# Optimization experiments

Hardware: AMD Instinct MI355X
Metric: run time of the kernel (lower is better)

The kernel has to match this reference:

```python
import jax, jax.numpy as jnp
import numpy as np

INV_SQRT3 = 0.5773502691896258  # e3nn wigner_3j entries for (0,1,1),(1,0,1),(1,1,0)


def setup_inputs() -> dict:
    key = jax.random.key(0)
    ks = jax.random.split(key, 9)
    B, N = 2, 256
    d_in, m1 = 256, 1          # input irreps: d_in x0e + m1 x1o
    d_h, m5, m3 = 256, 5, 3    # hidden irreps: d_h x0e + 5 x1o + 3 x1o
    d_out = 2                  # output irreps: 2 x0e
    return {
        "vectors": jax.random.normal(ks[0], (B, N, 3 * m1), jnp.float32),
        "scalars": jax.random.normal(ks[1], (B, N, d_in), jnp.float32),
        # e3nn internal weights ~ N(0,1); one weight block per CG path (uvw)
        "W1": jax.random.normal(ks[2], (d_in, d_in, d_h), jnp.float32),   # 0e x 0e -> 0e
        "W2a": jax.random.normal(ks[3], (d_in, m1, m5), jnp.float32),     # 0e x 1o -> 1o (mul 5)
        "W2b": jax.random.normal(ks[4], (d_in, m1, m3), jnp.float32),     # 0e x 1o -> 1o (mul 3)
        "W3a": jax.random.normal(ks[5], (m1, d_in, m5), jnp.float32),     # 1o x 0e -> 1o (mul 5)
        "W3b": jax.random.normal(ks[6], (m1, d_in, m3), jnp.float32),     # 1o x 0e -> 1o (mul 3)
        "W4": jax.random.normal(ks[7], (m1, m1, d_h), jnp.float32),       # 1o x 1o -> 0e
        "WL": jax.random.normal(ks[8], (d_h, d_out), jnp.float32),        # Linear d_h x0e -> 2 x0e
    }


def reference(vectors, scalars, W1, W2a, W2b, W3a, W3b, W4, WL):
    B, N, d = scalars.shape
    m1 = vectors.shape[-1] // 3
    z = B * N
    s = scalars.reshape(z, d)          # (z, d)  scalar (0e) channels
    v = vectors.reshape(z, m1, 3)      # (z, m1, 3)  vector (1o) channels
    d_h = W1.shape[-1]
    # e3nn FullyConnectedTensorProduct path weights ('component' irrep norm,
    # 'element' path norm): sqrt(ir_out.dim / sum_paths(mul1*mul2))
    pw0 = (1.0 / (d * d + m1 * m1)) ** 0.5      # into 0e output (paths 0e*0e and 1o*1o)
    pw1 = (3.0 / (2.0 * d * m1)) ** 0.5         # into each 1o output (paths 0e*1o and 1o*0e)
    # --- 0e x 0e -> 0e (dominant path) + 1o x 1o -> 0e ---
    t = jnp.einsum('zu,uvw->zvw', s, W1)        # (z, d, d_h)
    out0 = jnp.einsum('zv,zvw->zw', s, t)       # (z, d_h)
    out0 = out0 + INV_SQRT3 * jnp.einsum('zui,zvi,uvw->zw', v, v, W4)
    out0 = pw0 * out0
    # --- 0e x 1o -> 1o and 1o x 0e -> 1o (present in hidden irreps; they have
    # no path into the final 2x0e output, kept for structural fidelity) ---
    out1 = pw1 * INV_SQRT3 * (jnp.einsum('zu,zvk,uvw->zwk', s, v, W2a)
                              + jnp.einsum('zuk,zv,uvw->zwk', v, s, W3a))  # (z,5,3)
    out2 = pw1 * INV_SQRT3 * (jnp.einsum('zu,zvk,uvw->zwk', s, v, W2b)
                              + jnp.einsum('zuk,zv,uvw->zwk', v, s, W3b))  # (z,3,3)
    del out1, out2
    # --- e3nn Linear(hidden, 2x0e): only 0e->0e path, 1/sqrt(fan_in) norm ---
    lin = jnp.einsum('zu,uw->zw', out0, WL) / (d_h ** 0.5)   # (z, 2)
    m_eqv = lin[:, :1].reshape(B, N, 1)
    m_inv = lin[:, 1:].reshape(B, N, 1)
    return (m_eqv, m_inv)
```

## Files before the change

kernel.cpp:

```cpp
#include <hip/hip_runtime.h>


typedef __attribute__((ext_vector_type(8))) short bf16x8;
typedef __attribute__((ext_vector_type(4))) float f32x4;
typedef __attribute__((ext_vector_type(4))) int int4v;

#define LDS_S_BYTES 65536
#define LDS_B_PITCH 80
#define LDS_B_TILE (64 * LDS_B_PITCH)
#define LDS_TOTAL (LDS_S_BYTES + 2 * LDS_B_TILE)

__device__ __forceinline__ float bfbits2f(unsigned short h) {
  return __uint_as_float(((unsigned)h) << 16);
}
__device__ __forceinline__ unsigned pk2bf(float lo, float hi) {
  unsigned r;
  asm("v_cvt_pk_bf16_f32 %0, %1, %2" : "=v"(r) : "v"(lo), "v"(hi));
  return r;
}

__global__ __launch_bounds__(512) void eg_gemm(const float* __restrict__ s,
                                               const float* __restrict__ W1,
                                               float* __restrict__ out0) {
  extern __shared__ char smem[];
  char* sB0 = smem + LDS_S_BYTES;

  const int bx = blockIdx.x;
  const int nt = bx & 3;
  const int vc = (bx >> 2) & 7;
  const int uc = bx >> 5;
  const int u0 = uc * 32, v0 = vc * 32, w0 = nt * 64;

  const int tid = threadIdx.x;
  const int lane = tid & 63;
  const int wid = tid >> 6;
  const int l15 = lane & 15;
  const int g = lane >> 4;

  for (int j = 0; j < 16; ++j) {
    int id = j * 512 + tid;
    int z = id >> 4;
    int c4 = id & 15;
    int srccol = (c4 < 8) ? (u0 + (c4 << 2)) : (v0 + ((c4 - 8) << 2));
    const float4 f = *(const float4*)(s + z * 256 + srccol);
    unsigned p0 = pk2bf(f.x, f.y);
    unsigned p1 = pk2bf(f.z, f.w);
    int slot = c4 >> 1;
    char* dst = smem + z * 128 + (((slot ^ (z & 7)) << 4) | ((c4 & 1) << 3));
    *(unsigned*)dst = p0;
    *(unsigned*)(dst + 4) = p1;
  }

  const int vrow = tid >> 4;
  const int w4g = (tid & 15) << 2;
  const float* gsrc = W1 + (((u0 * 256) + v0 + vrow) * 256 + w0 + w4g);

  {
    float4 c0 = *(const float4*)(gsrc);
    unsigned q0 = pk2bf(c0.x, c0.y), q1 = pk2bf(c0.z, c0.w);
    char* base = sB0 + vrow * 2;
    *(unsigned short*)(base + (w4g + 0) * LDS_B_PITCH) = (unsigned short)(q0);
    *(unsigned short*)(base + (w4g + 1) * LDS_B_PITCH) = (unsigned short)(q0 >> 16);
    *(unsigned short*)(base + (w4g + 2) * LDS_B_PITCH) = (unsigned short)(q1);
    *(unsigned short*)(base + (w4g + 3) * LDS_B_PITCH) = (unsigned short)(q1 >> 16);
  }
  __syncthreads();

  f32x4 acc[4][4];
  #pragma unroll
  for (int a = 0; a < 4; ++a)
    #pragma unroll
    for (int b = 0; b < 4; ++b)
      acc[a][b] = 0.f;

  const int zb = wid * 64 + l15;
  const char* sbase = smem + zb * 128;
  const int svoff = ((4 + g) ^ (l15 & 7)) << 4;
  const int broff = l15 * LDS_B_PITCH + g * 16;

  for (int us = 0; us < 32; ++us) {
    float4 nx;
    if (us < 31) nx = *(const float4*)(gsrc + (us + 1) * 65536);

    const char* bt = sB0 + (us & 1) * LDS_B_TILE;

    bf16x8 afr[4];
    const int suoff = ((((us >> 3) ^ (l15 & 7)) << 4) | ((us & 7) << 1));
    #pragma unroll
    for (int mf = 0; mf < 4; ++mf) {
      const char* rowp = sbase + mf * 16 * 128;
      float su = bfbits2f(*(const unsigned short*)(rowp + suoff));
      int4v sv = *(const int4v*)(rowp + svoff);
      int4v af;
      #pragma unroll
      for (int jj = 0; jj < 4; ++jj) {
        unsigned p = (unsigned)sv[jj];
        float f0 = __uint_as_float(p << 16) * su;
        float f1 = __uint_as_float(p & 0xffff0000u) * su;
        af[jj] = (int)pk2bf(f0, f1);
      }
      afr[mf] = __builtin_bit_cast(bf16x8, af);
    }

    #pragma unroll
    for (int nf = 0; nf < 4; ++nf) {
      bf16x8 bfr = *(const bf16x8*)(bt + nf * 16 * LDS_B_PITCH + broff);
      #pragma unroll
      for (int mf = 0; mf < 4; ++mf) {
        acc[mf][nf] = __builtin_amdgcn_mfma_f32_16x16x32_bf16(afr[mf], bfr, acc[mf][nf], 0, 0, 0);
      }
    }

    if (us < 31) {
      char* btn = sB0 + ((us + 1) & 1) * LDS_B_TILE;
      unsigned q0 = pk2bf(nx.x, nx.y), q1 = pk2bf(nx.z, nx.w);
      char* base = btn + vrow * 2;
      *(unsigned short*)(base + (w4g + 0) * LDS_B_PITCH) = (unsigned short)(q0);
      *(unsigned short*)(base + (w4g + 1) * LDS_B_PITCH) = (unsigned short)(q0 >> 16);
      *(unsigned short*)(base + (w4g + 2) * LDS_B_PITCH) = (unsigned short)(q1);
      *(unsigned short*)(base + (w4g + 3) * LDS_B_PITCH) = (unsigned short)(q1 >> 16);
    }
    __syncthreads();
  }

  #pragma unroll
  for (int mf = 0; mf < 4; ++mf)
    #pragma unroll
    for (int nf = 0; nf < 4; ++nf)
      #pragma unroll
      for (int r = 0; r < 4; ++r) {
        int z = wid * 64 + mf * 16 + g * 4 + r;
        int w = w0 + nf * 16 + l15;
        atomicAdd(out0 + z * 256 + w, acc[mf][nf][r]);
      }
}

__global__ void eg_finish(const float* __restrict__ vec,
                          const float* __restrict__ W4,
                          const float* __restrict__ WL,
                          const float* __restrict__ acc,
                          float* __restrict__ out) {
  const int z = blockIdx.x;
  const int lane = threadIdx.x;
  float v0 = vec[z * 3 + 0], v1 = vec[z * 3 + 1], v2 = vec[z * 3 + 2];
  const float b = 0.57735026918962576f * (v0 * v0 + v1 * v1 + v2 * v2);
  float a0 = 0.f, a1 = 0.f;
  #pragma unroll
  for (int j = 0; j < 4; ++j) {
    int w = j * 64 + lane;
    float o = acc[z * 256 + w] + b * W4[w];
    a0 += o * WL[2 * w];
    a1 += o * WL[2 * w + 1];
  }
  #pragma unroll
  for (int off = 32; off > 0; off >>= 1) {
    a0 += __shfl_xor(a0, off);
    a1 += __shfl_xor(a1, off);
  }
  if (lane == 0) {
    out[z] = 2.4413876e-04f * a0;
    out[512 + z] = 2.4413876e-04f * a1;
  }
}

extern "C" void kernel_launch(void* const* d_in, const int* in_sizes, int n_in,
                              void* d_out, int out_size, void* d_ws, size_t ws_size,
                              hipStream_t stream) {
  const float* vectors = (const float*)d_in[0];
  const float* scalars = (const float*)d_in[1];
  const float* W1 = (const float*)d_in[2];
  const float* W4 = (const float*)d_in[7];
  const float* WL = (const float*)d_in[8];
  float* out = (float*)d_out;
  float* acc = (float*)d_ws;

  hipMemsetAsync(acc, 0, 512 * 256 * sizeof(float), stream);
  eg_gemm<<<256, 512, LDS_TOTAL, stream>>>(scalars, W1, acc);
  eg_finish<<<512, 64, 0, stream>>>(vectors, W4, WL, acc, out);
}
```

Baseline: 160.3 us.

## Switch GEMM to fp16, split z across blocks, deepen W1 prefetch pipeline

The kernel now converts operands to fp16 with round-toward-zero packing and uses f16 MFMA, so the per-step A-fragment scaling becomes packed half multiplies instead of unpack, fp32 multiply and repack. The grid goes from 256 blocks of 512 threads to 512 blocks of 256 threads, splitting z in two halves, which halves LDS per block and lets more blocks run per CU. W1 is prefetched two u-steps at a time through registers with a four-buffer LDS ring and swizzled vector writes, replacing the scattered 2-byte transposed stores, with a barrier every two steps instead of every step. fp16 products may lose range and precision, and each W1 tile is now loaded twice, once per z half.

```diff
diff --git a/kernel.cpp b/kernel.cpp
--- a/kernel.cpp
+++ b/kernel.cpp
@@ -1,137 +1,177 @@
 #include <hip/hip_runtime.h>
 
 
-typedef __attribute__((ext_vector_type(8))) short bf16x8;
+typedef __attribute__((ext_vector_type(8))) _Float16 f16x8;
+typedef __attribute__((ext_vector_type(2))) _Float16 f16x2;
 typedef __attribute__((ext_vector_type(4))) float f32x4;
+typedef __attribute__((ext_vector_type(2))) int int2v;
 typedef __attribute__((ext_vector_type(4))) int int4v;
 
-#define LDS_S_BYTES 65536
-#define LDS_B_PITCH 80
-#define LDS_B_TILE (64 * LDS_B_PITCH)
-#define LDS_TOTAL (LDS_S_BYTES + 2 * LDS_B_TILE)
-
-__device__ __forceinline__ float bfbits2f(unsigned short h) {
-  return __uint_as_float(((unsigned)h) << 16);
-}
-__device__ __forceinline__ unsigned pk2bf(float lo, float hi) {
-  unsigned r;
-  asm("v_cvt_pk_bf16_f32 %0, %1, %2" : "=v"(r) : "v"(lo), "v"(hi));
-  return r;
-}
-
-__global__ __launch_bounds__(512) void eg_gemm(const float* __restrict__ s,
-                                               const float* __restrict__ W1,
-                                               float* __restrict__ out0) {
+#define LDS_S 32768
+#define BP 80
+#define BSTEP 5120
+#define LDS_TOTAL (LDS_S + 4 * BSTEP)
+
+__device__ __forceinline__ unsigned pkrtz(float a, float b) {
+  return __builtin_bit_cast(unsigned, __builtin_amdgcn_cvt_pkrtz(a, b));
+}
+__device__ __forceinline__ int hbits(f16x2 h) {
+  return __builtin_bit_cast(int, h);
+}
+__device__ __forceinline__ void barrier_lds() {
+  asm volatile("s_waitcnt lgkmcnt(0)" ::: "memory");
+  __builtin_amdgcn_s_barrier();
+}
+
+__global__ __launch_bounds__(256, 3) void eg_gemm(const float* __restrict__ s,
+                                                  const float* __restrict__ W1,
+                                                  float* __restrict__ out0) {
   extern __shared__ char smem[];
-  char* sB0 = smem + LDS_S_BYTES;
+  char* sB = smem + LDS_S;
 
   const int bx = blockIdx.x;
-  const int nt = bx & 3;
-  const int vc = (bx >> 2) & 7;
-  const int uc = bx >> 5;
-  const int u0 = uc * 32, v0 = vc * 32, w0 = nt * 64;
-
-  const int tid = threadIdx.x;
-  const int lane = tid & 63;
-  const int wid = tid >> 6;
+  const int zh = bx >> 8;
+  const int uvw = bx & 255;
+  const int wt = uvw & 3, vc = (uvw >> 2) & 7, uc = uvw >> 5;
+  const int u0 = uc * 32, v0 = vc * 32, w0 = wt * 64;
+
+  const int t = threadIdx.x;
+  const int lane = t & 63;
+  const int wid = t >> 6;
   const int l15 = lane & 15;
   const int g = lane >> 4;
 
   for (int j = 0; j < 16; ++j) {
-    int id = j * 512 + tid;
-    int z = id >> 4;
+    int id = j * 256 + t;
+    int zl = id >> 4;
     int c4 = id & 15;
     int srccol = (c4 < 8) ? (u0 + (c4 << 2)) : (v0 + ((c4 - 8) << 2));
-    const float4 f = *(const float4*)(s + z * 256 + srccol);
-    unsigned p0 = pk2bf(f.x, f.y);
-    unsigned p1 = pk2bf(f.z, f.w);
+    const float4 f = *(const float4*)(s + (zh * 256 + zl) * 256 + srccol);
     int slot = c4 >> 1;
-    char* dst = smem + z * 128 + (((slot ^ (z & 7)) << 4) | ((c4 & 1) << 3));
-    *(unsigned*)dst = p0;
-    *(unsigned*)(dst + 4) = p1;
-  }
-
-  const int vrow = tid >> 4;
-  const int w4g = (tid & 15) << 2;
-  const float* gsrc = W1 + (((u0 * 256) + v0 + vrow) * 256 + w0 + w4g);
-
-  {
-    float4 c0 = *(const float4*)(gsrc);
-    unsigned q0 = pk2bf(c0.x, c0.y), q1 = pk2bf(c0.z, c0.w);
-    char* base = sB0 + vrow * 2;
-    *(unsigned short*)(base + (w4g + 0) * LDS_B_PITCH) = (unsigned short)(q0);
-    *(unsigned short*)(base + (w4g + 1) * LDS_B_PITCH) = (unsigned short)(q0 >> 16);
-    *(unsigned short*)(base + (w4g + 2) * LDS_B_PITCH) = (unsigned short)(q1);
-    *(unsigned short*)(base + (w4g + 3) * LDS_B_PITCH) = (unsigned short)(q1 >> 16);
-  }
-  __syncthreads();
+    char* dst = smem + zl * 128 + (((slot ^ (zl & 7)) << 4) | ((c4 & 1) << 3));
+    *(int2v*)dst = int2v{(int)pkrtz(f.x, f.y), (int)pkrtz(f.z, f.w)};
+  }
+
+  const int wB = t & 63;
+  const int vg = t >> 6;
+  const int hsw = (wB >> 3) & 7;
+  const int sl0 = (vg ^ hsw) << 3;
+  const int sl1 = ((vg + 4) ^ hsw) << 3;
+  const float* gB = W1 + (size_t)u0 * 65536 + (v0 + vg * 4) * 256 + w0 + wB;
+
+  float pa0, pa1, pa2, pa3, pa4, pa5, pa6, pa7;
+  float pb0, pb1, pb2, pb3, pb4, pb5, pb6, pb7;
+
+#define ISSUE(usbase)                                                       \
+  do {                                                                      \
+    const float* q0_ = gB + (size_t)(usbase) * 65536;                       \
+    pa0 = q0_[0];    pa1 = q0_[256];      pa2 = q0_[512];  pa3 = q0_[768];  \
+    pa4 = q0_[4096]; pa5 = q0_[4096+256]; pa6 = q0_[4096+512];              \
+    pa7 = q0_[4096+768];                                                    \
+    const float* q1_ = q0_ + 65536;                                         \
+    pb0 = q1_[0];    pb1 = q1_[256];      pb2 = q1_[512];  pb3 = q1_[768];  \
+    pb4 = q1_[4096]; pb5 = q1_[4096+256]; pb6 = q1_[4096+512];              \
+    pb7 = q1_[4096+768];                                                    \
+  } while (0)
+
+#define WRITEPF(dst0_)                                                       \
+  do {                                                                       \
+    char* d0_ = (dst0_);                                                     \
+    *(int2v*)(d0_ + wB * BP + sl0) =                                         \
+        int2v{(int)pkrtz(pa0, pa1), (int)pkrtz(pa2, pa3)};                   \
+    *(int2v*)(d0_ + wB * BP + sl1) =                                         \
+        int2v{(int)pkrtz(pa4, pa5), (int)pkrtz(pa6, pa7)};                   \
+    char* d1_ = d0_ + BSTEP;                                                 \
+    *(int2v*)(d1_ + wB * BP + sl0) =                                         \
+        int2v{(int)pkrtz(pb0, pb1), (int)pkrtz(pb2, pb3)};                   \
+    *(int2v*)(d1_ + wB * BP + sl1) =                                         \
+        int2v{(int)pkrtz(pb4, pb5), (int)pkrtz(pb6, pb7)};                   \
+  } while (0)
+
+  ISSUE(0);
+  WRITEPF(sB);
+  ISSUE(2);
+  barrier_lds();
+
+  const int swz = l15 & 7;
+  int4v sv[4];
+#pragma unroll
+  for (int mf = 0; mf < 4; ++mf) {
+    const char* p = smem + (wid * 64 + mf * 16 + l15) * 128 + (((4 + g) ^ swz) << 4);
+    sv[mf] = *(const int4v*)p;
+  }
+
+  int baddr[4];
+#pragma unroll
+  for (int nf = 0; nf < 4; ++nf) {
+    int w = nf * 16 + l15;
+    baddr[nf] = w * BP + (((2 * g) ^ ((w >> 3) & 7)) << 3);
+  }
 
   f32x4 acc[4][4];
-  #pragma unroll
+#pragma unroll
   for (int a = 0; a < 4; ++a)
-    #pragma unroll
-    for (int b = 0; b < 4; ++b)
-      acc[a][b] = 0.f;
-
-  const int zb = wid * 64 + l15;
-  const char* sbase = smem + zb * 128;
-  const int svoff = ((4 + g) ^ (l15 & 7)) << 4;
-  const int broff = l15 * LDS_B_PITCH + g * 16;
-
-  for (int us = 0; us < 32; ++us) {
-    float4 nx;
-    if (us < 31) nx = *(const float4*)(gsrc + (us + 1) * 65536);
-
-    const char* bt = sB0 + (us & 1) * LDS_B_TILE;
-
-    bf16x8 afr[4];
-    const int suoff = ((((us >> 3) ^ (l15 & 7)) << 4) | ((us & 7) << 1));
-    #pragma unroll
+#pragma unroll
+    for (int b = 0; b < 4; ++b) acc[a][b] = 0.f;
+
+  for (int q = 0; q < 8; ++q) {
+    int2v sur[4];
+#pragma unroll
     for (int mf = 0; mf < 4; ++mf) {
-      const char* rowp = sbase + mf * 16 * 128;
-      float su = bfbits2f(*(const unsigned short*)(rowp + suoff));
-      int4v sv = *(const int4v*)(rowp + svoff);
-      int4v af;
-      #pragma unroll
-      for (int jj = 0; jj < 4; ++jj) {
-        unsigned p = (unsigned)sv[jj];
-        float f0 = __uint_as_float(p << 16) * su;
-        float f1 = __uint_as_float(p & 0xffff0000u) * su;
-        af[jj] = (int)pk2bf(f0, f1);
+      const char* p = smem + (wid * 64 + mf * 16 + l15) * 128 +
+                      ((((q >> 1) ^ swz) << 4) | ((q & 1) << 3));
+      sur[mf] = *(const int2v*)p;
+    }
+#pragma unroll
+    for (int rr = 0; rr < 2; ++rr) {
+      const int r = 2 * q + rr;
+      const char* bufc = sB + rr * (2 * BSTEP);
+      char* bufn = sB + (rr ^ 1) * (2 * BSTEP);
+#pragma unroll
+      for (int p = 0; p < 2; ++p) {
+        f16x8 afr[4];
+#pragma unroll
+        for (int mf = 0; mf < 4; ++mf) {
+          unsigned dw = (unsigned)sur[mf][rr];
+          unsigned s2 = __builtin_amdgcn_perm(dw, dw, p ? 0x03020302u : 0x01000100u);
+          f16x2 su2 = __builtin_bit_cast(f16x2, s2);
+          int4v af;
+#pragma unroll
+          for (int jj = 0; jj < 4; ++jj) {
+            f16x2 pv = __builtin_bit_cast(f16x2, (unsigned)sv[mf][jj]);
+            f16x2 pr = su2 * pv;
+            af[jj] = hbits(pr);
+          }
+          afr[mf] = __builtin_bit_cast(f16x8, af);
+        }
+        const char* bp = bufc + p * BSTEP;
+#pragma unroll
+        for (int nf = 0; nf < 4; ++nf) {
+          int2v d0 = *(const int2v*)(bp + baddr[nf]);
+          int2v d1 = *(const int2v*)(bp + (baddr[nf] ^ 8));
+          int4v bf4 = int4v{d0[0], d0[1], d1[0], d1[1]};
+          f16x8 bfr = __builtin_bit_cast(f16x8, bf4);
+#pragma unroll
+          for (int mf = 0; mf < 4; ++mf)
+            acc[mf][nf] =
+                __builtin_amdgcn_mfma_f32_16x16x32_f16(afr[mf], bfr, acc[mf][nf], 0, 0, 0);
+        }
       }
-      afr[mf] = __builtin_bit_cast(bf16x8, af);
+      if (r < 15) WRITEPF(bufn);
+      if (r < 14) ISSUE(2 * (r + 2));
+      if (r < 15) barrier_lds();
     }
-
-    #pragma unroll
-    for (int nf = 0; nf < 4; ++nf) {
-      bf16x8 bfr = *(const bf16x8*)(bt + nf * 16 * LDS_B_PITCH + broff);
-      #pragma unroll
-      for (int mf = 0; mf < 4; ++mf) {
-        acc[mf][nf] = __builtin_amdgcn_mfma_f32_16x16x32_bf16(afr[mf], bfr, acc[mf][nf], 0, 0, 0);
-      }
-    }
-
-    if (us < 31) {
-      char* btn = sB0 + ((us + 1) & 1) * LDS_B_TILE;
-      unsigned q0 = pk2bf(nx.x, nx.y), q1 = pk2bf(nx.z, nx.w);
-      char* base = btn + vrow * 2;
-      *(unsigned short*)(base + (w4g + 0) * LDS_B_PITCH) = (unsigned short)(q0);
-      *(unsigned short*)(base + (w4g + 1) * LDS_B_PITCH) = (unsigned short)(q0 >> 16);
-      *(unsigned short*)(base + (w4g + 2) * LDS_B_PITCH) = (unsigned short)(q1);
-      *(unsigned short*)(base + (w4g + 3) * LDS_B_PITCH) = (unsigned short)(q1 >> 16);
-    }
-    __syncthreads();
-  }
-
-  #pragma unroll
+  }
+
+#pragma unroll
   for (int mf = 0; mf < 4; ++mf)
-    #pragma unroll
+#pragma unroll
     for (int nf = 0; nf < 4; ++nf)
-      #pragma unroll
-      for (int r = 0; r < 4; ++r) {
-        int z = wid * 64 + mf * 16 + g * 4 + r;
+#pragma unroll
+      for (int rI = 0; rI < 4; ++rI) {
+        int z = zh * 256 + wid * 64 + mf * 16 + g * 4 + rI;
         int w = w0 + nf * 16 + l15;
-        atomicAdd(out0 + z * 256 + w, acc[mf][nf][r]);
+        atomicAdd(out0 + z * 256 + w, acc[mf][nf][rI]);
       }
 }
 
@@ -145,14 +185,14 @@
   float v0 = vec[z * 3 + 0], v1 = vec[z * 3 + 1], v2 = vec[z * 3 + 2];
   const float b = 0.57735026918962576f * (v0 * v0 + v1 * v1 + v2 * v2);
   float a0 = 0.f, a1 = 0.f;
-  #pragma unroll
+#pragma unroll
   for (int j = 0; j < 4; ++j) {
     int w = j * 64 + lane;
     float o = acc[z * 256 + w] + b * W4[w];
     a0 += o * WL[2 * w];
     a1 += o * WL[2 * w + 1];
   }
-  #pragma unroll
+#pragma unroll
   for (int off = 32; off > 0; off >>= 1) {
     a0 += __shfl_xor(a0, off);
     a1 += __shfl_xor(a1, off);
@@ -174,7 +214,7 @@
   float* out = (float*)d_out;
   float* acc = (float*)d_ws;
 
-  hipMemsetAsync(acc, 0, 512 * 256 * sizeof(float), stream);
-  eg_gemm<<<256, 512, LDS_TOTAL, stream>>>(scalars, W1, acc);
+  (void)hipMemsetAsync(acc, 0, 512 * 256 * sizeof(float), stream);
+  eg_gemm<<<512, 256, LDS_TOTAL, stream>>>(scalars, W1, acc);
   eg_finish<<<512, 64, 0, stream>>>(vectors, W4, WL, acc, out);
 }
```

Result: slower. 166.7 us (+4.0%).
